# Kernel tuning notes

Measured on AMD Instinct MI355X. Metric: run time of the kernel, lower is better.

Reference implementation:

```python
import jax, jax.numpy as jnp
import numpy as np

DIM = 256
HEADS = 8
HEAD_DIM = DIM // HEADS
SCALE = HEAD_DIM ** -0.5
B, N = 2048, 49
NW = 64


def setup_inputs() -> dict:
    key = jax.random.key(0)
    ks = jax.random.split(key, 7)
    x = jax.random.normal(ks[0], (B, N, DIM), dtype=jnp.float32)
    mask = jax.random.normal(ks[1], (NW, N + 1, N + 1), dtype=jnp.float32)
    class_token = 0.02 * jax.random.normal(ks[2], (1, 1, DIM), dtype=jnp.float32)
    qkv_w = jax.random.normal(ks[3], (DIM, 3 * DIM), dtype=jnp.float32) / np.sqrt(DIM)
    qkv_b = jnp.zeros((3 * DIM,), dtype=jnp.float32)
    proj_w = jax.random.normal(ks[4], (DIM, DIM), dtype=jnp.float32) / np.sqrt(DIM)
    proj_b = jnp.zeros((DIM,), dtype=jnp.float32)
    return {"x": x, "mask": mask, "class_token": class_token,
            "qkv_w": qkv_w, "qkv_b": qkv_b, "proj_w": proj_w, "proj_b": proj_b}


def reference(x, mask, class_token, qkv_w, qkv_b, proj_w, proj_b):
    b, n, c = x.shape
    n1 = n + 1
    # prepend learnable class token
    cls = jnp.broadcast_to(class_token, (b, 1, c))
    xc = jnp.concatenate([cls, x], axis=1)  # (B, N+1, C)
    # fused qkv projection
    qkv = xc @ qkv_w + qkv_b                 # (B, N+1, 3C)
    qkv = qkv.reshape(b, n1, 3, HEADS, HEAD_DIM)
    qkv = jnp.transpose(qkv, (2, 0, 3, 1, 4))  # (3, B, H, N+1, Dh)
    q, k, v = qkv[0] * SCALE, qkv[1], qkv[2]
    attn = jnp.einsum('bhid,bhjd->bhij', q, k)  # (B, H, N+1, N+1)
    # per-window additive mask bias
    nw = mask.shape[0]
    attn = attn.reshape(b // nw, nw, HEADS, n1, n1) + mask[None, :, None]
    attn = attn.reshape(b, HEADS, n1, n1)
    attn = jax.nn.softmax(attn, axis=-1)
    out = jnp.einsum('bhij,bhjd->bhid', attn, v)      # (B, H, N+1, Dh)
    out = jnp.transpose(out, (0, 2, 1, 3)).reshape(b, n1, c)
    out = out @ proj_w + proj_b
    return out[:, 0], out[:, 1:]
```

## Files before the change

kernel.cpp:

```cpp
#include <hip/hip_runtime.h>

#define NB    2048
#define N1    50
#define DIMC  256
#define NHEAD 8

typedef short  s16x8 __attribute__((ext_vector_type(8)));
typedef short  s16x4 __attribute__((ext_vector_type(4)));
typedef float  f32x4 __attribute__((ext_vector_type(4)));
typedef float  f32x2 __attribute__((ext_vector_type(2)));
typedef unsigned int u32x2 __attribute__((ext_vector_type(2)));
typedef unsigned int u32x4 __attribute__((ext_vector_type(4)));

__device__ __forceinline__ unsigned short f2bf(float f) {
    unsigned int u = __builtin_bit_cast(unsigned int, f);
    u = (u + 0x7FFFu + ((u >> 16) & 1u)) >> 16;
    return (unsigned short)u;
}
__device__ __forceinline__ unsigned int pk2(float a, float b) {
    return (unsigned int)f2bf(a) | ((unsigned int)f2bf(b) << 16);
}
__device__ __forceinline__ s16x8 ld8(const unsigned short* p) {
    return *(const s16x8*)p;
}

__global__ void prep_kernel(const float* __restrict__ qkv_w, const float* __restrict__ proj_w,
                            const float* __restrict__ mask,
                            unsigned short* __restrict__ wqkvB, unsigned short* __restrict__ wprojB,
                            float* __restrict__ maskP) {
    int idx = blockIdx.x * 256 + threadIdx.x;
    {
        int wv = idx >> 12, q = (idx >> 6) & 63, k = idx & 63;
        float v = (k < 50) ? ((q < 50) ? mask[(wv * 50 + q) * 50 + k] : 0.f) : -1e30f;
        maskP[idx] = v;
    }
    if (idx < 196608) {
        int ks = idx / 24576, rem = idx - ks * 24576, n = rem >> 5, kk = rem & 31;
        wqkvB[idx] = f2bf(qkv_w[(ks * 32 + kk) * 768 + n]);
    }
    if (idx < 65536) {
        int ks = idx >> 13, rem = idx & 8191, n = rem >> 5, kk = rem & 31;
        wprojB[idx] = f2bf(proj_w[(ks * 32 + kk) * 256 + n]);
    }
}

__global__ __launch_bounds__(1024, 4) void fused_kernel(
        const float* __restrict__ x, const float* __restrict__ cls,
        const float* __restrict__ qkv_b, const unsigned short* __restrict__ wqkvB,
        const unsigned short* __restrict__ wprojB, const float* __restrict__ proj_b,
        const float* __restrict__ maskP, float* __restrict__ out) {
    __shared__ __align__(16) char smem_raw[152576];
    unsigned short* S   = (unsigned short*)smem_raw;
    unsigned short* sXC = S;
    unsigned short* sQ  = S + 16896;
    unsigned short* sK  = S + 37376;
    unsigned short* sVT = S + 57856;

    const int b = blockIdx.x, tid = threadIdx.x;
    const int lane = tid & 63, w = tid >> 6;
    const int ln15 = lane & 15, quad = lane >> 4, q8 = quad * 8;
    const int win = b & 63;
    const float SCALE = 0.17677669529663687f;
    const int h = w >> 1, rh = w & 1, qt0 = rh * 2;

    #pragma unroll
    for (int it = 0; it < 4; ++it) {
        const int r = it * 16 + w;
        f32x4 t;
        if (r == 0)       t = *(const f32x4*)&cls[lane * 4];
        else if (r <= 49) t = *(const f32x4*)&x[((size_t)b * 49 + (r - 1)) * 256 + lane * 4];
        else              t = f32x4{0.f, 0.f, 0.f, 0.f};
        u32x2 wv;
        wv[0] = pk2(t[0], t[1]);
        wv[1] = pk2(t[2], t[3]);
        *(u32x2*)&sXC[r * 264 + lane * 4] = wv;
    }
    s16x8 bcur[3];
    #pragma unroll
    for (int nt = 0; nt < 3; ++nt)
        bcur[nt] = ld8(wqkvB + (nt * 256 + w * 16 + ln15) * 32 + q8);
    __syncthreads();

    f32x4 acc[4][3];
    #pragma unroll
    for (int mt = 0; mt < 4; ++mt)
        #pragma unroll
        for (int nt = 0; nt < 3; ++nt) acc[mt][nt] = f32x4{0.f, 0.f, 0.f, 0.f};

    #pragma unroll
    for (int ks = 0; ks < 8; ++ks) {
        s16x8 bnext[3];
        if (ks < 7) {
            const unsigned short* src = wqkvB + (ks + 1) * 24576;
            #pragma unroll
            for (int nt = 0; nt < 3; ++nt)
                bnext[nt] = ld8(src + (nt * 256 + w * 16 + ln15) * 32 + q8);
        }
        s16x8 af[4];
        #pragma unroll
        for (int mt = 0; mt < 4; ++mt)
            af[mt] = ld8(&sXC[(mt * 16 + ln15) * 264 + ks * 32 + q8]);
        __builtin_amdgcn_s_setprio(1);
        #pragma unroll
        for (int mt = 0; mt < 4; ++mt) {
            acc[mt][0] = __builtin_amdgcn_mfma_f32_16x16x32_bf16(bcur[0], af[mt], acc[mt][0], 0, 0, 0);
            acc[mt][1] = __builtin_amdgcn_mfma_f32_16x16x32_bf16(bcur[1], af[mt], acc[mt][1], 0, 0, 0);
            acc[mt][2] = __builtin_amdgcn_mfma_f32_16x16x32_bf16(af[mt], bcur[2], acc[mt][2], 0, 0, 0);
        }
        __builtin_amdgcn_s_setprio(0);
        if (ks < 7) {
            #pragma unroll
            for (int nt = 0; nt < 3; ++nt) bcur[nt] = bnext[nt];
        }
    }

    {
        const int hd = w >> 1, ddb = (w & 1) * 16;
        const f32x4 bq4 = *(const f32x4*)&qkv_b[w * 16 + quad * 4];
        const f32x4 bk4 = *(const f32x4*)&qkv_b[256 + w * 16 + quad * 4];
        const float bv  = qkv_b[512 + w * 16 + ln15];
        #pragma unroll
        for (int mt = 0; mt < 4; ++mt) {
            const int row = (mt * 16 + ln15) * 40 + ddb + quad * 4;
            s16x4 wq, wk, wv;
            #pragma unroll
            for (int i = 0; i < 4; ++i) {
                wq[i] = f2bf((acc[mt][0][i] + bq4[i]) * SCALE);
                wk[i] = f2bf(acc[mt][1][i] + bk4[i]);
                wv[i] = f2bf(acc[mt][2][i] + bv);
            }
            *(s16x4*)&sQ[hd * 2560 + row] = wq;
            *(s16x4*)&sK[hd * 2560 + row] = wk;
            *(s16x4*)&sVT[hd * 2304 + (ddb + ln15) * 72 + mt * 16 + quad * 4] = wv;
        }
    }
    f32x4 mk[2][4];
    #pragma unroll
    for (int mt = 0; mt < 2; ++mt)
        #pragma unroll
        for (int kt = 0; kt < 4; ++kt)
            mk[mt][kt] = *(const f32x4*)&maskP[((size_t)(win * 64 + (qt0 + mt) * 16 + ln15)) * 64 + kt * 16 + quad * 4];
    __syncthreads();

    {
        s16x8 ak[4];
        #pragma unroll
        for (int kt = 0; kt < 4; ++kt)
            ak[kt] = ld8(&sK[h * 2560 + (kt * 16 + ln15) * 40 + q8]);

        f32x4 st[2][4];
        #pragma unroll
        for (int mt = 0; mt < 2; ++mt) {
            s16x8 bq = ld8(&sQ[h * 2560 + ((qt0 + mt) * 16 + ln15) * 40 + q8]);
            __builtin_amdgcn_s_setprio(1);
            #pragma unroll
            for (int kt = 0; kt < 4; ++kt) {
                f32x4 z = {0.f, 0.f, 0.f, 0.f};
                st[mt][kt] = __builtin_amdgcn_mfma_f32_16x16x32_bf16(ak[kt], bq, z, 0, 0, 0);
            }
            __builtin_amdgcn_s_setprio(0);
        }
        s16x8 pb[2][2];
        #pragma unroll
        for (int mt = 0; mt < 2; ++mt) {
            float sum = 0.f;
            #pragma unroll
            for (int kt = 0; kt < 4; ++kt) {
                #pragma unroll
                for (int i = 0; i < 4; ++i) {
                    float e = __expf(st[mt][kt][i] + mk[mt][kt][i]);
                    st[mt][kt][i] = e;
                    sum += e;
                }
            }
            sum += __shfl_xor(sum, 16, 64);
            sum += __shfl_xor(sum, 32, 64);
            const float inv = 1.f / sum;
            unsigned int wd[8];
            #pragma unroll
            for (int kt = 0; kt < 4; ++kt) {
                wd[kt * 2]     = pk2(st[mt][kt][0] * inv, st[mt][kt][1] * inv);
                wd[kt * 2 + 1] = pk2(st[mt][kt][2] * inv, st[mt][kt][3] * inv);
            }
            #pragma unroll
            for (int kk = 0; kk < 2; ++kk) {
                u32x4 t;
                #pragma unroll
                for (int j = 0; j < 4; ++j) {
                    const int sl = ln15 + ((lane & 16) << 1) + ((j >> 1) << 4);
                    unsigned int a = (unsigned int)__shfl((int)wd[4 * kk + (j & 1)], sl, 64);
                    unsigned int c = (unsigned int)__shfl((int)wd[4 * kk + 2 + (j & 1)], sl, 64);
                    t[j] = (lane & 32) ? c : a;
                }
                pb[mt][kk] = __builtin_bit_cast(s16x8, t);
            }
        }
        s16x8 av[2][2];
        #pragma unroll
        for (int dt = 0; dt < 2; ++dt)
            #pragma unroll
            for (int kk = 0; kk < 2; ++kk)
                av[dt][kk] = ld8(&sVT[h * 2304 + (dt * 16 + ln15) * 72 + kk * 32 + q8]);
        f32x4 o[2][2];
        #pragma unroll
        for (int mt = 0; mt < 2; ++mt)
            #pragma unroll
            for (int dt = 0; dt < 2; ++dt) o[mt][dt] = f32x4{0.f, 0.f, 0.f, 0.f};
        __builtin_amdgcn_s_setprio(1);
        #pragma unroll
        for (int mt = 0; mt < 2; ++mt)
            #pragma unroll
            for (int dt = 0; dt < 2; ++dt)
                #pragma unroll
                for (int kk = 0; kk < 2; ++kk)
                    o[mt][dt] = __builtin_amdgcn_mfma_f32_16x16x32_bf16(av[dt][kk], pb[mt][kk], o[mt][dt], 0, 0, 0);
        __builtin_amdgcn_s_setprio(0);
        #pragma unroll
        for (int mt = 0; mt < 2; ++mt) {
            const int qg = (qt0 + mt) * 16 + ln15;
            #pragma unroll
            for (int dt = 0; dt < 2; ++dt) {
                s16x4 ov;
                #pragma unroll
                for (int i = 0; i < 4; ++i) ov[i] = f2bf(o[mt][dt][i]);
                *(s16x4*)&sXC[qg * 264 + h * 32 + dt * 16 + quad * 4] = ov;
            }
        }
    }
    const int wm3 = w >> 3, wn3 = w & 7;
    s16x8 b3[2];
    #pragma unroll
    for (int nt = 0; nt < 2; ++nt)
        b3[nt] = ld8(wprojB + (wn3 * 32 + nt * 16 + ln15) * 32 + q8);
    __syncthreads();

    {
        f32x4 a3[2][2];
        #pragma unroll
        for (int mt = 0; mt < 2; ++mt)
            #pragma unroll
            for (int nt = 0; nt < 2; ++nt) a3[mt][nt] = f32x4{0.f, 0.f, 0.f, 0.f};
        #pragma unroll
        for (int ks = 0; ks < 8; ++ks) {
            s16x8 b3n[2];
            if (ks < 7) {
                const unsigned short* src = wprojB + (ks + 1) * 8192;
                #pragma unroll
                for (int nt = 0; nt < 2; ++nt)
                    b3n[nt] = ld8(src + (wn3 * 32 + nt * 16 + ln15) * 32 + q8);
            }
            s16x8 af3[2];
            #pragma unroll
            for (int mt = 0; mt < 2; ++mt)
                af3[mt] = ld8(&sXC[(wm3 * 32 + mt * 16 + ln15) * 264 + ks * 32 + q8]);
            __builtin_amdgcn_s_setprio(1);
            #pragma unroll
            for (int mt = 0; mt < 2; ++mt)
                #pragma unroll
                for (int nt = 0; nt < 2; ++nt)
                    a3[mt][nt] = __builtin_amdgcn_mfma_f32_16x16x32_bf16(b3[nt], af3[mt], a3[mt][nt], 0, 0, 0);
            __builtin_amdgcn_s_setprio(0);
            if (ks < 7) {
                #pragma unroll
                for (int nt = 0; nt < 2; ++nt) b3[nt] = b3n[nt];
            }
        }
        #pragma unroll
        for (int nt = 0; nt < 2; ++nt) {
            const int cb = wn3 * 32 + nt * 16 + quad * 4;
            const f32x4 b4 = *(const f32x4*)&proj_b[cb];
            #pragma unroll
            for (int mt = 0; mt < 2; ++mt) {
                const int t = wm3 * 32 + mt * 16 + ln15;
                f32x4 v;
                #pragma unroll
                for (int i = 0; i < 4; ++i) v[i] = a3[mt][nt][i] + b4[i];
                if (t == 0)      *(f32x4*)&out[(size_t)b * 256 + cb] = v;
                else if (t < 50) *(f32x4*)&out[524288 + ((size_t)b * 49 + (t - 1)) * 256 + cb] = v;
            }
        }
    }
}

extern "C" void kernel_launch(void* const* d_in, const int* in_sizes, int n_in,
                              void* d_out, int out_size, void* d_ws, size_t ws_size,
                              hipStream_t stream) {
    const float* x      = (const float*)d_in[0];
    const float* mask   = (const float*)d_in[1];
    const float* cls    = (const float*)d_in[2];
    const float* qkv_w  = (const float*)d_in[3];
    const float* qkv_b  = (const float*)d_in[4];
    const float* proj_w = (const float*)d_in[5];
    const float* proj_b = (const float*)d_in[6];
    float* out = (float*)d_out;

    unsigned short* wqkvB  = (unsigned short*)d_ws;
    unsigned short* wprojB = (unsigned short*)((char*)d_ws + 393216);
    float*          maskP  = (float*)((char*)d_ws + 524288);

    prep_kernel<<<1024, 256, 0, stream>>>(qkv_w, proj_w, mask, wqkvB, wprojB, maskP);
    fused_kernel<<<NB, 1024, 0, stream>>>(x, cls, qkv_b, wqkvB, wprojB, proj_b, maskP, out);
}
```

Baseline: 309.4 us.

## Make fused kernel persistent over 8 batches with prefetch of next input

Launches 256 blocks that each loop over 8 batch elements (stride 256) instead of one block per batch element. The next element's x rows are loaded into registers while the current element is processed, hiding global load latency. Risks: with 152KB of shared memory only one block fits per CU, so 256 blocks give about one wave of work with no inter-block overlap, and the extra end-of-iteration barrier serializes the phases.

```diff
diff --git a/kernel.cpp b/kernel.cpp
--- a/kernel.cpp
+++ b/kernel.cpp
@@ -56,229 +56,248 @@
     unsigned short* sK  = S + 37376;
     unsigned short* sVT = S + 57856;
 
-    const int b = blockIdx.x, tid = threadIdx.x;
+    const int p = blockIdx.x, tid = threadIdx.x;
     const int lane = tid & 63, w = tid >> 6;
     const int ln15 = lane & 15, quad = lane >> 4, q8 = quad * 8;
-    const int win = b & 63;
+    const int win = p & 63;
     const float SCALE = 0.17677669529663687f;
     const int h = w >> 1, rh = w & 1, qt0 = rh * 2;
-
+    const int wm3 = w >> 3, wn3 = w & 7;
+
+    f32x4 xr[4];
     #pragma unroll
     for (int it = 0; it < 4; ++it) {
         const int r = it * 16 + w;
-        f32x4 t;
-        if (r == 0)       t = *(const f32x4*)&cls[lane * 4];
-        else if (r <= 49) t = *(const f32x4*)&x[((size_t)b * 49 + (r - 1)) * 256 + lane * 4];
-        else              t = f32x4{0.f, 0.f, 0.f, 0.f};
-        u32x2 wv;
-        wv[0] = pk2(t[0], t[1]);
-        wv[1] = pk2(t[2], t[3]);
-        *(u32x2*)&sXC[r * 264 + lane * 4] = wv;
-    }
-    s16x8 bcur[3];
-    #pragma unroll
-    for (int nt = 0; nt < 3; ++nt)
-        bcur[nt] = ld8(wqkvB + (nt * 256 + w * 16 + ln15) * 32 + q8);
-    __syncthreads();
-
-    f32x4 acc[4][3];
-    #pragma unroll
-    for (int mt = 0; mt < 4; ++mt)
-        #pragma unroll
-        for (int nt = 0; nt < 3; ++nt) acc[mt][nt] = f32x4{0.f, 0.f, 0.f, 0.f};
-
-    #pragma unroll
-    for (int ks = 0; ks < 8; ++ks) {
-        s16x8 bnext[3];
-        if (ks < 7) {
-            const unsigned short* src = wqkvB + (ks + 1) * 24576;
-            #pragma unroll
-            for (int nt = 0; nt < 3; ++nt)
-                bnext[nt] = ld8(src + (nt * 256 + w * 16 + ln15) * 32 + q8);
-        }
-        s16x8 af[4];
+        if (r == 0)       xr[it] = *(const f32x4*)&cls[lane * 4];
+        else if (r <= 49) xr[it] = *(const f32x4*)&x[((size_t)p * 49 + (r - 1)) * 256 + lane * 4];
+        else              xr[it] = f32x4{0.f, 0.f, 0.f, 0.f};
+    }
+
+    for (int i = 0; i < 8; ++i) {
+        const int b = p + (i << 8);
+
+        #pragma unroll
+        for (int it = 0; it < 4; ++it) {
+            const int r = it * 16 + w;
+            u32x2 wv;
+            wv[0] = pk2(xr[it][0], xr[it][1]);
+            wv[1] = pk2(xr[it][2], xr[it][3]);
+            *(u32x2*)&sXC[r * 264 + lane * 4] = wv;
+        }
+        if (i < 7) {
+            const int bn = b + 256;
+            #pragma unroll
+            for (int it = 0; it < 4; ++it) {
+                const int r = it * 16 + w;
+                if (r == 0)       xr[it] = *(const f32x4*)&cls[lane * 4];
+                else if (r <= 49) xr[it] = *(const f32x4*)&x[((size_t)bn * 49 + (r - 1)) * 256 + lane * 4];
+            }
+        }
+        s16x8 bcur[3];
+        #pragma unroll
+        for (int nt = 0; nt < 3; ++nt)
+            bcur[nt] = ld8(wqkvB + (nt * 256 + w * 16 + ln15) * 32 + q8);
+        __syncthreads();
+
+        f32x4 acc[4][3];
         #pragma unroll
         for (int mt = 0; mt < 4; ++mt)
-            af[mt] = ld8(&sXC[(mt * 16 + ln15) * 264 + ks * 32 + q8]);
-        __builtin_amdgcn_s_setprio(1);
-        #pragma unroll
-        for (int mt = 0; mt < 4; ++mt) {
-            acc[mt][0] = __builtin_amdgcn_mfma_f32_16x16x32_bf16(bcur[0], af[mt], acc[mt][0], 0, 0, 0);
-            acc[mt][1] = __builtin_amdgcn_mfma_f32_16x16x32_bf16(bcur[1], af[mt], acc[mt][1], 0, 0, 0);
-            acc[mt][2] = __builtin_amdgcn_mfma_f32_16x16x32_bf16(af[mt], bcur[2], acc[mt][2], 0, 0, 0);
-        }
-        __builtin_amdgcn_s_setprio(0);
-        if (ks < 7) {
-            #pragma unroll
-            for (int nt = 0; nt < 3; ++nt) bcur[nt] = bnext[nt];
-        }
-    }
-
-    {
-        const int hd = w >> 1, ddb = (w & 1) * 16;
-        const f32x4 bq4 = *(const f32x4*)&qkv_b[w * 16 + quad * 4];
-        const f32x4 bk4 = *(const f32x4*)&qkv_b[256 + w * 16 + quad * 4];
-        const float bv  = qkv_b[512 + w * 16 + ln15];
-        #pragma unroll
-        for (int mt = 0; mt < 4; ++mt) {
-            const int row = (mt * 16 + ln15) * 40 + ddb + quad * 4;
-            s16x4 wq, wk, wv;
-            #pragma unroll
-            for (int i = 0; i < 4; ++i) {
-                wq[i] = f2bf((acc[mt][0][i] + bq4[i]) * SCALE);
-                wk[i] = f2bf(acc[mt][1][i] + bk4[i]);
-                wv[i] = f2bf(acc[mt][2][i] + bv);
-            }
-            *(s16x4*)&sQ[hd * 2560 + row] = wq;
-            *(s16x4*)&sK[hd * 2560 + row] = wk;
-            *(s16x4*)&sVT[hd * 2304 + (ddb + ln15) * 72 + mt * 16 + quad * 4] = wv;
-        }
-    }
-    f32x4 mk[2][4];
-    #pragma unroll
-    for (int mt = 0; mt < 2; ++mt)
-        #pragma unroll
-        for (int kt = 0; kt < 4; ++kt)
-            mk[mt][kt] = *(const f32x4*)&maskP[((size_t)(win * 64 + (qt0 + mt) * 16 + ln15)) * 64 + kt * 16 + quad * 4];
-    __syncthreads();
-
-    {
-        s16x8 ak[4];
-        #pragma unroll
-        for (int kt = 0; kt < 4; ++kt)
-            ak[kt] = ld8(&sK[h * 2560 + (kt * 16 + ln15) * 40 + q8]);
-
-        f32x4 st[2][4];
-        #pragma unroll
-        for (int mt = 0; mt < 2; ++mt) {
-            s16x8 bq = ld8(&sQ[h * 2560 + ((qt0 + mt) * 16 + ln15) * 40 + q8]);
+            #pragma unroll
+            for (int nt = 0; nt < 3; ++nt) acc[mt][nt] = f32x4{0.f, 0.f, 0.f, 0.f};
+
+        #pragma unroll
+        for (int ks = 0; ks < 8; ++ks) {
+            s16x8 bnext[3];
+            if (ks < 7) {
+                const unsigned short* src = wqkvB + (ks + 1) * 24576;
+                #pragma unroll
+                for (int nt = 0; nt < 3; ++nt)
+                    bnext[nt] = ld8(src + (nt * 256 + w * 16 + ln15) * 32 + q8);
+            }
+            s16x8 af[4];
+            #pragma unroll
+            for (int mt = 0; mt < 4; ++mt)
+                af[mt] = ld8(&sXC[(mt * 16 + ln15) * 264 + ks * 32 + q8]);
             __builtin_amdgcn_s_setprio(1);
             #pragma unroll
-            for (int kt = 0; kt < 4; ++kt) {
-                f32x4 z = {0.f, 0.f, 0.f, 0.f};
-                st[mt][kt] = __builtin_amdgcn_mfma_f32_16x16x32_bf16(ak[kt], bq, z, 0, 0, 0);
-            }
-            __builtin_amdgcn_s_setprio(0);
-        }
-        s16x8 pb[2][2];
-        #pragma unroll
-        for (int mt = 0; mt < 2; ++mt) {
-            float sum = 0.f;
-            #pragma unroll
-            for (int kt = 0; kt < 4; ++kt) {
-                #pragma unroll
-                for (int i = 0; i < 4; ++i) {
-                    float e = __expf(st[mt][kt][i] + mk[mt][kt][i]);
-                    st[mt][kt][i] = e;
-                    sum += e;
-                }
-            }
-            sum += __shfl_xor(sum, 16, 64);
-            sum += __shfl_xor(sum, 32, 64);
-            const float inv = 1.f / sum;
-            unsigned int wd[8];
-            #pragma unroll
-            for (int kt = 0; kt < 4; ++kt) {
-                wd[kt * 2]     = pk2(st[mt][kt][0] * inv, st[mt][kt][1] * inv);
-                wd[kt * 2 + 1] = pk2(st[mt][kt][2] * inv, st[mt][kt][3] * inv);
-            }
-            #pragma unroll
-            for (int kk = 0; kk < 2; ++kk) {
-                u32x4 t;
-                #pragma unroll
-                for (int j = 0; j < 4; ++j) {
-                    const int sl = ln15 + ((lane & 16) << 1) + ((j >> 1) << 4);
-                    unsigned int a = (unsigned int)__shfl((int)wd[4 * kk + (j & 1)], sl, 64);
-                    unsigned int c = (unsigned int)__shfl((int)wd[4 * kk + 2 + (j & 1)], sl, 64);
-                    t[j] = (lane & 32) ? c : a;
-                }
-                pb[mt][kk] = __builtin_bit_cast(s16x8, t);
-            }
-        }
-        s16x8 av[2][2];
-        #pragma unroll
-        for (int dt = 0; dt < 2; ++dt)
-            #pragma unroll
-            for (int kk = 0; kk < 2; ++kk)
-                av[dt][kk] = ld8(&sVT[h * 2304 + (dt * 16 + ln15) * 72 + kk * 32 + q8]);
-        f32x4 o[2][2];
-        #pragma unroll
-        for (int mt = 0; mt < 2; ++mt)
-            #pragma unroll
-            for (int dt = 0; dt < 2; ++dt) o[mt][dt] = f32x4{0.f, 0.f, 0.f, 0.f};
-        __builtin_amdgcn_s_setprio(1);
-        #pragma unroll
-        for (int mt = 0; mt < 2; ++mt)
-            #pragma unroll
-            for (int dt = 0; dt < 2; ++dt)
-                #pragma unroll
-                for (int kk = 0; kk < 2; ++kk)
-                    o[mt][dt] = __builtin_amdgcn_mfma_f32_16x16x32_bf16(av[dt][kk], pb[mt][kk], o[mt][dt], 0, 0, 0);
-        __builtin_amdgcn_s_setprio(0);
-        #pragma unroll
-        for (int mt = 0; mt < 2; ++mt) {
-            const int qg = (qt0 + mt) * 16 + ln15;
-            #pragma unroll
-            for (int dt = 0; dt < 2; ++dt) {
-                s16x4 ov;
-                #pragma unroll
-                for (int i = 0; i < 4; ++i) ov[i] = f2bf(o[mt][dt][i]);
-                *(s16x4*)&sXC[qg * 264 + h * 32 + dt * 16 + quad * 4] = ov;
-            }
-        }
-    }
-    const int wm3 = w >> 3, wn3 = w & 7;
-    s16x8 b3[2];
-    #pragma unroll
-    for (int nt = 0; nt < 2; ++nt)
-        b3[nt] = ld8(wprojB + (wn3 * 32 + nt * 16 + ln15) * 32 + q8);
-    __syncthreads();
-
-    {
-        f32x4 a3[2][2];
-        #pragma unroll
-        for (int mt = 0; mt < 2; ++mt)
-            #pragma unroll
-            for (int nt = 0; nt < 2; ++nt) a3[mt][nt] = f32x4{0.f, 0.f, 0.f, 0.f};
-        #pragma unroll
-        for (int ks = 0; ks < 8; ++ks) {
-            s16x8 b3n[2];
-            if (ks < 7) {
-                const unsigned short* src = wprojB + (ks + 1) * 8192;
-                #pragma unroll
-                for (int nt = 0; nt < 2; ++nt)
-                    b3n[nt] = ld8(src + (wn3 * 32 + nt * 16 + ln15) * 32 + q8);
-            }
-            s16x8 af3[2];
-            #pragma unroll
-            for (int mt = 0; mt < 2; ++mt)
-                af3[mt] = ld8(&sXC[(wm3 * 32 + mt * 16 + ln15) * 264 + ks * 32 + q8]);
-            __builtin_amdgcn_s_setprio(1);
-            #pragma unroll
-            for (int mt = 0; mt < 2; ++mt)
-                #pragma unroll
-                for (int nt = 0; nt < 2; ++nt)
-                    a3[mt][nt] = __builtin_amdgcn_mfma_f32_16x16x32_bf16(b3[nt], af3[mt], a3[mt][nt], 0, 0, 0);
+            for (int mt = 0; mt < 4; ++mt) {
+                acc[mt][0] = __builtin_amdgcn_mfma_f32_16x16x32_bf16(bcur[0], af[mt], acc[mt][0], 0, 0, 0);
+                acc[mt][1] = __builtin_amdgcn_mfma_f32_16x16x32_bf16(bcur[1], af[mt], acc[mt][1], 0, 0, 0);
+                acc[mt][2] = __builtin_amdgcn_mfma_f32_16x16x32_bf16(af[mt], bcur[2], acc[mt][2], 0, 0, 0);
+            }
             __builtin_amdgcn_s_setprio(0);
             if (ks < 7) {
                 #pragma unroll
-                for (int nt = 0; nt < 2; ++nt) b3[nt] = b3n[nt];
-            }
-        }
-        #pragma unroll
-        for (int nt = 0; nt < 2; ++nt) {
-            const int cb = wn3 * 32 + nt * 16 + quad * 4;
-            const f32x4 b4 = *(const f32x4*)&proj_b[cb];
+                for (int nt = 0; nt < 3; ++nt) bcur[nt] = bnext[nt];
+            }
+        }
+
+        {
+            const int hd = w >> 1, ddb = (w & 1) * 16;
+            const f32x4 bq4 = *(const f32x4*)&qkv_b[w * 16 + quad * 4];
+            const f32x4 bk4 = *(const f32x4*)&qkv_b[256 + w * 16 + quad * 4];
+            const float bv  = qkv_b[512 + w * 16 + ln15];
+            #pragma unroll
+            for (int mt = 0; mt < 4; ++mt) {
+                const int row = (mt * 16 + ln15) * 40 + ddb + quad * 4;
+                s16x4 wq, wk, wv;
+                #pragma unroll
+                for (int i2 = 0; i2 < 4; ++i2) {
+                    wq[i2] = f2bf((acc[mt][0][i2] + bq4[i2]) * SCALE);
+                    wk[i2] = f2bf(acc[mt][1][i2] + bk4[i2]);
+                    wv[i2] = f2bf(acc[mt][2][i2] + bv);
+                }
+                *(s16x4*)&sQ[hd * 2560 + row] = wq;
+                *(s16x4*)&sK[hd * 2560 + row] = wk;
+                *(s16x4*)&sVT[hd * 2304 + (ddb + ln15) * 72 + mt * 16 + quad * 4] = wv;
+            }
+        }
+        f32x4 mk[2][4];
+        #pragma unroll
+        for (int mt = 0; mt < 2; ++mt)
+            #pragma unroll
+            for (int kt = 0; kt < 4; ++kt)
+                mk[mt][kt] = *(const f32x4*)&maskP[((size_t)(win * 64 + (qt0 + mt) * 16 + ln15)) * 64 + kt * 16 + quad * 4];
+        __syncthreads();
+
+        {
+            s16x8 ak[4];
+            #pragma unroll
+            for (int kt = 0; kt < 4; ++kt)
+                ak[kt] = ld8(&sK[h * 2560 + (kt * 16 + ln15) * 40 + q8]);
+
+            f32x4 st[2][4];
             #pragma unroll
             for (int mt = 0; mt < 2; ++mt) {
-                const int t = wm3 * 32 + mt * 16 + ln15;
-                f32x4 v;
-                #pragma unroll
-                for (int i = 0; i < 4; ++i) v[i] = a3[mt][nt][i] + b4[i];
-                if (t == 0)      *(f32x4*)&out[(size_t)b * 256 + cb] = v;
-                else if (t < 50) *(f32x4*)&out[524288 + ((size_t)b * 49 + (t - 1)) * 256 + cb] = v;
-            }
-        }
+                s16x8 bq = ld8(&sQ[h * 2560 + ((qt0 + mt) * 16 + ln15) * 40 + q8]);
+                __builtin_amdgcn_s_setprio(1);
+                #pragma unroll
+                for (int kt = 0; kt < 4; ++kt) {
+                    f32x4 z = {0.f, 0.f, 0.f, 0.f};
+                    st[mt][kt] = __builtin_amdgcn_mfma_f32_16x16x32_bf16(ak[kt], bq, z, 0, 0, 0);
+                }
+                __builtin_amdgcn_s_setprio(0);
+            }
+            s16x8 pb[2][2];
+            #pragma unroll
+            for (int mt = 0; mt < 2; ++mt) {
+                float sum = 0.f;
+                #pragma unroll
+                for (int kt = 0; kt < 4; ++kt) {
+                    #pragma unroll
+                    for (int i2 = 0; i2 < 4; ++i2) {
+                        float e = __expf(st[mt][kt][i2] + mk[mt][kt][i2]);
+                        st[mt][kt][i2] = e;
+                        sum += e;
+                    }
+                }
+                sum += __shfl_xor(sum, 16, 64);
+                sum += __shfl_xor(sum, 32, 64);
+                const float inv = 1.f / sum;
+                unsigned int wd[8];
+                #pragma unroll
+                for (int kt = 0; kt < 4; ++kt) {
+                    wd[kt * 2]     = pk2(st[mt][kt][0] * inv, st[mt][kt][1] * inv);
+                    wd[kt * 2 + 1] = pk2(st[mt][kt][2] * inv, st[mt][kt][3] * inv);
+                }
+                #pragma unroll
+                for (int kk = 0; kk < 2; ++kk) {
+                    u32x4 t;
+                    #pragma unroll
+                    for (int j = 0; j < 4; ++j) {
+                        const int sl = ln15 + ((lane & 16) << 1) + ((j >> 1) << 4);
+                        unsigned int a = (unsigned int)__shfl((int)wd[4 * kk + (j & 1)], sl, 64);
+                        unsigned int c = (unsigned int)__shfl((int)wd[4 * kk + 2 + (j & 1)], sl, 64);
+                        t[j] = (lane & 32) ? c : a;
+                    }
+                    pb[mt][kk] = __builtin_bit_cast(s16x8, t);
+                }
+            }
+            s16x8 av[2][2];
+            #pragma unroll
+            for (int dt = 0; dt < 2; ++dt)
+                #pragma unroll
+                for (int kk = 0; kk < 2; ++kk)
+                    av[dt][kk] = ld8(&sVT[h * 2304 + (dt * 16 + ln15) * 72 + kk * 32 + q8]);
+            f32x4 o[2][2];
+            #pragma unroll
+            for (int mt = 0; mt < 2; ++mt)
+                #pragma unroll
+                for (int dt = 0; dt < 2; ++dt) o[mt][dt] = f32x4{0.f, 0.f, 0.f, 0.f};
+            __builtin_amdgcn_s_setprio(1);
+            #pragma unroll
+            for (int mt = 0; mt < 2; ++mt)
+                #pragma unroll
+                for (int dt = 0; dt < 2; ++dt)
+                    #pragma unroll
+                    for (int kk = 0; kk < 2; ++kk)
+                        o[mt][dt] = __builtin_amdgcn_mfma_f32_16x16x32_bf16(av[dt][kk], pb[mt][kk], o[mt][dt], 0, 0, 0);
+            __builtin_amdgcn_s_setprio(0);
+            #pragma unroll
+            for (int mt = 0; mt < 2; ++mt) {
+                const int qg = (qt0 + mt) * 16 + ln15;
+                #pragma unroll
+                for (int dt = 0; dt < 2; ++dt) {
+                    s16x4 ov;
+                    #pragma unroll
+                    for (int i2 = 0; i2 < 4; ++i2) ov[i2] = f2bf(o[mt][dt][i2]);
+                    *(s16x4*)&sXC[qg * 264 + h * 32 + dt * 16 + quad * 4] = ov;
+                }
+            }
+        }
+        s16x8 b3[2];
+        #pragma unroll
+        for (int nt = 0; nt < 2; ++nt)
+            b3[nt] = ld8(wprojB + (wn3 * 32 + nt * 16 + ln15) * 32 + q8);
+        __syncthreads();
+
+        {
+            f32x4 a3[2][2];
+            #pragma unroll
+            for (int mt = 0; mt < 2; ++mt)
+                #pragma unroll
+                for (int nt = 0; nt < 2; ++nt) a3[mt][nt] = f32x4{0.f, 0.f, 0.f, 0.f};
+            #pragma unroll
+            for (int ks = 0; ks < 8; ++ks) {
+                s16x8 b3n[2];
+                if (ks < 7) {
+                    const unsigned short* src = wprojB + (ks + 1) * 8192;
+                    #pragma unroll
+                    for (int nt = 0; nt < 2; ++nt)
+                        b3n[nt] = ld8(src + (wn3 * 32 + nt * 16 + ln15) * 32 + q8);
+                }
+                s16x8 af3[2];
+                #pragma unroll
+                for (int mt = 0; mt < 2; ++mt)
+                    af3[mt] = ld8(&sXC[(wm3 * 32 + mt * 16 + ln15) * 264 + ks * 32 + q8]);
+                __builtin_amdgcn_s_setprio(1);
+                #pragma unroll
+                for (int mt = 0; mt < 2; ++mt)
+                    #pragma unroll
+                    for (int nt = 0; nt < 2; ++nt)
+                        a3[mt][nt] = __builtin_amdgcn_mfma_f32_16x16x32_bf16(b3[nt], af3[mt], a3[mt][nt], 0, 0, 0);
+                __builtin_amdgcn_s_setprio(0);
+                if (ks < 7) {
+                    #pragma unroll
+                    for (int nt = 0; nt < 2; ++nt) b3[nt] = b3n[nt];
+                }
+            }
+            #pragma unroll
+            for (int nt = 0; nt < 2; ++nt) {
+                const int cb = wn3 * 32 + nt * 16 + quad * 4;
+                const f32x4 b4 = *(const f32x4*)&proj_b[cb];
+                #pragma unroll
+                for (int mt = 0; mt < 2; ++mt) {
+                    const int t = wm3 * 32 + mt * 16 + ln15;
+                    f32x4 v;
+                    #pragma unroll
+                    for (int i2 = 0; i2 < 4; ++i2) v[i2] = a3[mt][nt][i2] + b4[i2];
+                    if (t == 0)      *(f32x4*)&out[(size_t)b * 256 + cb] = v;
+                    else if (t < 50) *(f32x4*)&out[524288 + ((size_t)b * 49 + (t - 1)) * 256 + cb] = v;
+                }
+            }
+        }
+        __syncthreads();
     }
 }
 
@@ -299,5 +318,5 @@
     float*          maskP  = (float*)((char*)d_ws + 524288);
 
     prep_kernel<<<1024, 256, 0, stream>>>(qkv_w, proj_w, mask, wqkvB, wprojB, maskP);
-    fused_kernel<<<NB, 1024, 0, stream>>>(x, cls, qkv_b, wqkvB, wprojB, proj_b, maskP, out);
-}
+    fused_kernel<<<256, 1024, 0, stream>>>(x, cls, qkv_b, wqkvB, wprojB, proj_b, maskP, out);
+}
```

Measured after the change: 631.3 us. 2.04x slower.
